# Kernel optimization log

Hardware: AMD Instinct MI355X
Metric: run time of the kernel (lower is better)

## Reference

```python
import jax, jax.numpy as jnp
import numpy as np

T, B, I, H, L, D = 512, 64, 128, 256, 6, 2
G = 3 * H  # gates r, z, n (torch order)


def setup_inputs() -> dict:
    key = jax.random.key(0)
    ks = jax.random.split(key, 10)
    stdv = 1.0 / np.sqrt(H)
    u = lambda k, shp: jax.random.uniform(k, shp, jnp.float32, -stdv, stdv)
    return {
        "x": jax.random.normal(ks[0], (T, B, I), jnp.float32),
        "h0": jax.random.normal(ks[1], (L * D, B, H), jnp.float32),
        "w_ih0": u(ks[2], (D, G, I)),
        "w_hh0": u(ks[3], (D, G, H)),
        "b_ih0": u(ks[4], (D, G)),
        "b_hh0": u(ks[5], (D, G)),
        "w_ihr": u(ks[6], (L - 1, D, G, D * H)),
        "w_hhr": u(ks[7], (L - 1, D, G, H)),
        "b_ihr": u(ks[8], (L - 1, D, G)),
        "b_hhr": u(ks[9], (L - 1, D, G)),
    }


def _gru_direction(xg, h0, w_hh, b_hh, reverse):
    # xg: [T,B,3H] precomputed input-gate projections; h0: [B,H]
    if reverse:
        xg = xg[::-1]

    def step(h, xg_t):
        hg = h @ w_hh.T + b_hh                      # [B,3H]
        xr, xz, xn = jnp.split(xg_t, 3, axis=-1)
        hr, hz, hn = jnp.split(hg, 3, axis=-1)
        r = jax.nn.sigmoid(xr + hr)
        z = jax.nn.sigmoid(xz + hz)
        n = jnp.tanh(xn + r * hn)
        h_new = (1.0 - z) * n + z * h
        return h_new, h_new

    hT, ys = jax.lax.scan(step, h0, xg)
    if reverse:
        ys = ys[::-1]
    return ys, hT


def reference(x, h0, w_ih0, w_hh0, b_ih0, b_hh0, w_ihr, w_hhr, b_ihr, b_hhr):
    out = x
    h_n = []
    for layer in range(L):
        dir_outs = []
        for d in range(D):
            if layer == 0:
                w_ih, w_hh = w_ih0[d], w_hh0[d]
                b_ih, b_hh = b_ih0[d], b_hh0[d]
            else:
                w_ih, w_hh = w_ihr[layer - 1, d], w_hhr[layer - 1, d]
                b_ih, b_hh = b_ihr[layer - 1, d], b_hhr[layer - 1, d]
            # one big GEMM over the whole sequence for the input projection
            xg = jnp.einsum('tbi,gi->tbg', out, w_ih) + b_ih  # [T,B,3H]
            ys, hT = _gru_direction(xg, h0[layer * D + d], w_hh, b_hh,
                                    reverse=(d == 1))
            dir_outs.append(ys)
            h_n.append(hT)
        out = jnp.concatenate(dir_outs, axis=-1)  # [T,B,2H]
    return out, jnp.stack(h_n)  # ([T,B,2H], [L*D,B,H])
```

## Files before the change

kernel.cpp:

```cpp
#include <hip/hip_runtime.h>
#include <hip/hip_fp16.h>

typedef short bf16x8 __attribute__((ext_vector_type(8)));
typedef float f32x4  __attribute__((ext_vector_type(4)));
typedef _Float16 h2_t __attribute__((ext_vector_type(2)));

#define T_ 512
#define B_ 64
#define I_ 128
#define H_ 256
#define L_ 6
#define M_ 32768

static constexpr size_t XG_OFF    = 0;
static constexpr size_t X0_OFF    = 100663296;
static constexpr size_t YA_OFF    = 109051904;
static constexpr size_t YB_OFF    = 142606336;
static constexpr size_t WIH0_OFF  = 176160768;
static constexpr size_t WIHR_OFF  = 176553984;
static constexpr size_t WSCAN_OFF = 184418304;
static constexpr size_t BIAS_OFF  = 189136896;

__global__ void cvt_bf16(const float* __restrict__ s, unsigned short* __restrict__ d, int n) {
  for (int i = blockIdx.x * blockDim.x + threadIdx.x; i < n; i += gridDim.x * blockDim.x) {
    unsigned u = __builtin_bit_cast(unsigned, s[i]);
    u += 0x7fffu + ((u >> 16) & 1u);
    d[i] = (unsigned short)(u >> 16);
  }
}

__global__ void prep_wscan(const float* __restrict__ whh0, const float* __restrict__ whhr,
                           unsigned int* __restrict__ out) {
  int idx = blockIdx.x * 256 + threadIdx.x;
  int ld  = idx / 98304;
  int rem = idx - ld * 98304;
  int tg  = rem >> 15;
  int r   = (rem >> 8) & 127;
  int j   = rem & 255;
  const float* src = (ld < 2) ? (whh0 + (size_t)ld * 196608) : (whhr + (size_t)(ld - 2) * 196608);
  const float* row = src + (size_t)(tg * 256 + j) * 256;
  h2_t p; p[0] = (_Float16)row[2 * r]; p[1] = (_Float16)row[2 * r + 1];
  out[idx] = __builtin_bit_cast(unsigned int, p);
}

__global__ void prep_bias(const float* __restrict__ bih0, const float* __restrict__ bhh0,
                          const float* __restrict__ bihr, const float* __restrict__ bhhr,
                          float* __restrict__ out) {
  int idx = blockIdx.x * 256 + threadIdx.x;
  int ld = idx >> 10;
  int c  = (idx >> 8) & 3;
  int j  = idx & 255;
  const float* bi = (ld < 2) ? bih0 + ld * 768 : bihr + (ld - 2) * 768;
  const float* bh = (ld < 2) ? bhh0 + ld * 768 : bhhr + (ld - 2) * 768;
  float v;
  if (c == 0)      v = bi[j] + bh[j];
  else if (c == 1) v = bi[256 + j] + bh[256 + j];
  else if (c == 2) v = bi[512 + j];
  else             v = bh[512 + j];
  out[idx] = v;
}

__device__ __forceinline__ void llds16(const void* g, void* l) {
  __builtin_amdgcn_global_load_lds((const __attribute__((address_space(1))) void*)g,
                                   (__attribute__((address_space(3))) void*)l, 16, 0, 0);
}

__global__ __launch_bounds__(256)
void gemm_bt(const unsigned short* __restrict__ A,
             const unsigned short* __restrict__ Wl,
             __half* __restrict__ xg,
             int K) {
  const int m0 = blockIdx.x * 128;
  const int n0 = blockIdx.y * 128;
  const int d  = blockIdx.z;
  const unsigned short* W = Wl + (size_t)d * 768 * K;
  __half* C = xg + (size_t)d * M_ * 768;

  __shared__ short As[128 * 64];
  __shared__ short Bs[128 * 64];

  const int tid  = threadIdx.x;
  const int lane = tid & 63;

  const int wv = tid >> 6;
  const int wm = wv >> 1, wn = wv & 1;

  f32x4 acc[4][4] = {};

  for (int kt = 0; kt < K; kt += 64) {
#pragma unroll
    for (int i = 0; i < 4; i++) {
      int e = i * 256 + tid;
      int r = e >> 3, c = (e & 7) << 3;
      llds16(A + (size_t)(m0 + r) * K + kt + c, &As[e * 8]);
    }
#pragma unroll
    for (int i = 0; i < 4; i++) {
      int e = i * 256 + tid;
      int r = e >> 3, c = (e & 7) << 3;
      llds16(W + (size_t)(n0 + r) * K + kt + c, &Bs[e * 8]);
    }
    __syncthreads();
#pragma unroll
    for (int kf = 0; kf < 2; ++kf) {
      bf16x8 a[4], b[4];
      const int krow = kf * 32 + ((lane >> 4) << 3);
#pragma unroll
      for (int f = 0; f < 4; ++f)
        a[f] = *(const bf16x8*)&As[(wm * 64 + f * 16 + (lane & 15)) * 64 + krow];
#pragma unroll
      for (int f = 0; f < 4; ++f)
        b[f] = *(const bf16x8*)&Bs[(wn * 64 + f * 16 + (lane & 15)) * 64 + krow];
#pragma unroll
      for (int i = 0; i < 4; i++)
#pragma unroll
        for (int jn = 0; jn < 4; jn++)
          acc[i][jn] = __builtin_amdgcn_mfma_f32_16x16x32_bf16(a[i], b[jn], acc[i][jn], 0, 0, 0);
    }
    __syncthreads();
  }
#pragma unroll
  for (int i = 0; i < 4; i++) {
    const int row_b = m0 + wm * 64 + i * 16 + ((lane >> 4) << 2);
#pragma unroll
    for (int jn = 0; jn < 4; jn++) {
      const int col = n0 + wn * 64 + jn * 16 + (lane & 15);
#pragma unroll
      for (int v = 0; v < 4; ++v)
        C[(size_t)(row_b + v) * 768 + col] = __float2half(acc[i][jn][v]);
    }
  }
}

#define FDOT2(a, b, c) __builtin_amdgcn_fdot2((a), (b), (c), false)

__device__ __forceinline__ float dpp_xor1(float x) {
  int r = __builtin_amdgcn_update_dpp(0, __builtin_bit_cast(int, x), 0xB1, 0xF, 0xF, true);
  return __builtin_bit_cast(float, r);
}

__global__ __launch_bounds__(512, 2)
void gru_scan2(const unsigned int* __restrict__ wscan,
               const float* __restrict__ bias4,
               const __half* __restrict__ xg,
               const float* __restrict__ h0,
               unsigned short* __restrict__ yout,
               float* __restrict__ dout,
               int layer, int last) {
  const int tid  = threadIdx.x;
  const int j    = tid >> 1;
  const int half = tid & 1;
  const int b    = blockIdx.x;
  const int d    = blockIdx.y;
  const int ld   = layer * 2 + d;

  unsigned int wr[64], wz[64], wn_[64];
  {
    const unsigned int* wb = wscan + (size_t)ld * 98304 + (size_t)half * 64 * 256 + j;
#pragma unroll
    for (int r = 0; r < 64; r++) wr[r]  = wb[r * 256];
#pragma unroll
    for (int r = 0; r < 64; r++) wz[r]  = wb[32768 + r * 256];
#pragma unroll
    for (int r = 0; r < 64; r++) wn_[r] = wb[65536 + r * 256];
  }
  const float* bb = bias4 + ld * 1024;
  const float bR = bb[j], bZ = bb[256 + j], bXn = bb[512 + j], bHn = bb[768 + j];

  __shared__ __attribute__((aligned(16))) unsigned short hb[2][256];

  float h = h0[(size_t)ld * 16384 + b * 256 + j];
  if (half == 0) hb[0][j] = __half_as_ushort(__float2half(h));

  const __half* xgd = xg + (size_t)d * M_ * 768;
  const int t0 = d ? 511 : 0;
  size_t xb = (size_t)(t0 * 64 + b) * 768 + j;
  __half cxr = xgd[xb], cxz = xgd[xb + 256], cxn = xgd[xb + 512];

  __syncthreads();

  for (int s = 0; s < 512; s++) {
    const int cur = s & 1;
    const int sn = (s + 1) & 511;
    const int t1 = d ? 511 - sn : sn;
    const size_t xb1 = (size_t)(t1 * 64 + b) * 768 + j;
    const __half nxr = xgd[xb1], nxz = xgd[xb1 + 256], nxn = xgd[xb1 + 512];

    float ar = 0.f, az = 0.f, an = 0.f;
    const uint4* hp = (const uint4*)(&hb[cur][half << 7]);
#pragma unroll
    for (int q = 0; q < 16; q++) {
      const uint4 hv = hp[q];
      const h2_t p0 = __builtin_bit_cast(h2_t, hv.x);
      const h2_t p1 = __builtin_bit_cast(h2_t, hv.y);
      const h2_t p2 = __builtin_bit_cast(h2_t, hv.z);
      const h2_t p3 = __builtin_bit_cast(h2_t, hv.w);
      ar = FDOT2(p0, __builtin_bit_cast(h2_t, wr[4 * q + 0]), ar);
      az = FDOT2(p0, __builtin_bit_cast(h2_t, wz[4 * q + 0]), az);
      an = FDOT2(p0, __builtin_bit_cast(h2_t, wn_[4 * q + 0]), an);
      ar = FDOT2(p1, __builtin_bit_cast(h2_t, wr[4 * q + 1]), ar);
      az = FDOT2(p1, __builtin_bit_cast(h2_t, wz[4 * q + 1]), az);
      an = FDOT2(p1, __builtin_bit_cast(h2_t, wn_[4 * q + 1]), an);
      ar = FDOT2(p2, __builtin_bit_cast(h2_t, wr[4 * q + 2]), ar);
      az = FDOT2(p2, __builtin_bit_cast(h2_t, wz[4 * q + 2]), az);
      an = FDOT2(p2, __builtin_bit_cast(h2_t, wn_[4 * q + 2]), an);
      ar = FDOT2(p3, __builtin_bit_cast(h2_t, wr[4 * q + 3]), ar);
      az = FDOT2(p3, __builtin_bit_cast(h2_t, wz[4 * q + 3]), az);
      an = FDOT2(p3, __builtin_bit_cast(h2_t, wn_[4 * q + 3]), an);
    }
    ar += dpp_xor1(ar);
    az += dpp_xor1(az);
    an += dpp_xor1(an);

    const float prer = ar + __half2float(cxr) + bR;
    const float prez = az + __half2float(cxz) + bZ;
    const float r = __builtin_amdgcn_rcpf(1.f + __builtin_amdgcn_exp2f(-1.44269504f * prer));
    const float z = __builtin_amdgcn_rcpf(1.f + __builtin_amdgcn_exp2f(-1.44269504f * prez));
    const float pren = __half2float(cxn) + bXn + r * (an + bHn);
    const float e2 = __builtin_amdgcn_exp2f(2.88539008f * pren);
    const float n = 1.f - 2.f * __builtin_amdgcn_rcpf(e2 + 1.f);
    h = n + z * (h - n);

    if (half == 0) {
      hb[cur ^ 1][j] = __half_as_ushort(__float2half(h));
      const int t = d ? 511 - s : s;
      const size_t orow = (size_t)(t * 64 + b) * 512 + (size_t)d * 256 + j;
      if (last) {
        dout[orow] = h;
      } else {
        unsigned u = __builtin_bit_cast(unsigned, h);
        u += 0x7fffu + ((u >> 16) & 1u);
        yout[orow] = (unsigned short)(u >> 16);
      }
    }
    cxr = nxr; cxz = nxz; cxn = nxn;
    __syncthreads();
  }
  if (half == 0) dout[16777216 + (size_t)ld * 16384 + b * 256 + j] = h;
}

extern "C" void kernel_launch(void* const* d_in, const int* in_sizes, int n_in,
                              void* d_out, int out_size, void* d_ws, size_t ws_size,
                              hipStream_t stream) {
  const float* x    = (const float*)d_in[0];
  const float* h0   = (const float*)d_in[1];
  const float* wih0 = (const float*)d_in[2];
  const float* whh0 = (const float*)d_in[3];
  const float* bih0 = (const float*)d_in[4];
  const float* bhh0 = (const float*)d_in[5];
  const float* wihr = (const float*)d_in[6];
  const float* whhr = (const float*)d_in[7];
  const float* bihr = (const float*)d_in[8];
  const float* bhhr = (const float*)d_in[9];

  char* ws = (char*)d_ws;
  __half*        xg    = (__half*)(ws + XG_OFF);
  unsigned short* x0   = (unsigned short*)(ws + X0_OFF);
  unsigned short* yA   = (unsigned short*)(ws + YA_OFF);
  unsigned short* yB   = (unsigned short*)(ws + YB_OFF);
  unsigned short* wih0b= (unsigned short*)(ws + WIH0_OFF);
  unsigned short* wihrb= (unsigned short*)(ws + WIHR_OFF);
  unsigned int*  wscan = (unsigned int*)(ws + WSCAN_OFF);
  float*         bias4 = (float*)(ws + BIAS_OFF);
  float*         dout  = (float*)d_out;

  cvt_bf16<<<4096, 256, 0, stream>>>(x, x0, M_ * I_);
  cvt_bf16<<<768, 256, 0, stream>>>(wih0, wih0b, 2 * 768 * 128);
  cvt_bf16<<<4096, 256, 0, stream>>>(wihr, wihrb, 5 * 2 * 768 * 512);
  prep_wscan<<<4608, 256, 0, stream>>>(whh0, whhr, wscan);
  prep_bias<<<48, 256, 0, stream>>>(bih0, bhh0, bihr, bhhr, bias4);

  for (int l = 0; l < L_; l++) {
    unsigned short* yw = (l & 1) ? yB : yA;
    const unsigned short* A = (l == 0) ? x0 : ((l & 1) ? yA : yB);
    const int K = (l == 0) ? 128 : 512;
    const unsigned short* W = (l == 0) ? wih0b : wihrb + (size_t)(l - 1) * 2 * 768 * 512;

    gemm_bt<<<dim3(256, 6, 2), 256, 0, stream>>>(A, W, xg, K);
    gru_scan2<<<dim3(64, 2), 512, 0, stream>>>(wscan, bias4, xg, h0, yw, dout, l, l == L_ - 1);
  }
}
```

Before: 3.802 ms.

## Split recurrent weights between LDS and registers in GRU scan kernel

The recurrent weight slice per thread was held entirely in 192 VGPRs. It now keeps 40 rows per gate in registers and puts the first 24 rows per gate (144KB) in LDS. The hidden-state buffer is also XOR-swizzled so the two halves of a thread pair read different LDS banks. Launch bounds drop to one block per CU to match the LDS footprint. The aim is to cut register pressure or spilling in the serial time loop, at the cost of extra LDS reads on every step.

```diff
diff --git a/kernel.cpp b/kernel.cpp
--- a/kernel.cpp
+++ b/kernel.cpp
@@ -133,13 +133,14 @@
 }
 
 #define FDOT2(a, b, c) __builtin_amdgcn_fdot2((a), (b), (c), false)
+#define BC2(u) __builtin_bit_cast(h2_t, (u))
 
 __device__ __forceinline__ float dpp_xor1(float x) {
   int r = __builtin_amdgcn_update_dpp(0, __builtin_bit_cast(int, x), 0xB1, 0xF, 0xF, true);
   return __builtin_bit_cast(float, r);
 }
 
-__global__ __launch_bounds__(512, 2)
+__global__ __launch_bounds__(512, 1)
 void gru_scan2(const unsigned int* __restrict__ wscan,
                const float* __restrict__ bias4,
                const __half* __restrict__ xg,
@@ -154,30 +155,51 @@
   const int d    = blockIdx.y;
   const int ld   = layer * 2 + d;
 
-  unsigned int wr[64], wz[64], wn_[64];
-  {
-    const unsigned int* wb = wscan + (size_t)ld * 98304 + (size_t)half * 64 * 256 + j;
-#pragma unroll
-    for (int r = 0; r < 64; r++) wr[r]  = wb[r * 256];
-#pragma unroll
-    for (int r = 0; r < 64; r++) wz[r]  = wb[32768 + r * 256];
-#pragma unroll
-    for (int r = 0; r < 64; r++) wn_[r] = wb[65536 + r * 256];
-  }
+  __shared__ unsigned int wlds[36864];
+  __shared__ __attribute__((aligned(16))) char hbc[2][512];
+
+  const unsigned int* wb = wscan + (size_t)ld * 98304 + (size_t)half * 16384 + j;
+
+#pragma unroll
+  for (int g = 0; g < 3; g++)
+#pragma unroll
+    for (int rr = 0; rr < 24; rr++)
+      wlds[g * 12288 + rr * 512 + tid] = wb[g * 32768 + rr * 256];
+
+  unsigned int wr[40], wz[40], wn_[40];
+#pragma unroll
+  for (int i = 0; i < 40; i++) wr[i]  = wb[(24 + i) * 256];
+#pragma unroll
+  for (int i = 0; i < 40; i++) wz[i]  = wb[32768 + (24 + i) * 256];
+#pragma unroll
+  for (int i = 0; i < 40; i++) wn_[i] = wb[65536 + (24 + i) * 256];
+#pragma unroll
+  for (int i = 0; i < 40; i++) {
+    asm volatile("" : "+v"(wr[i]));
+    asm volatile("" : "+v"(wz[i]));
+    asm volatile("" : "+v"(wn_[i]));
+  }
+
   const float* bb = bias4 + ld * 1024;
   const float bR = bb[j], bZ = bb[256 + j], bXn = bb[512 + j], bHn = bb[768 + j];
 
-  __shared__ __attribute__((aligned(16))) unsigned short hb[2][256];
+  const int wboff = (j * 2) ^ ((j & 128) >> 3);
 
   float h = h0[(size_t)ld * 16384 + b * 256 + j];
-  if (half == 0) hb[0][j] = __half_as_ushort(__float2half(h));
+  if (half == 0) *(unsigned short*)(hbc[0] + wboff) = __half_as_ushort(__float2half(h));
 
   const __half* xgd = xg + (size_t)d * M_ * 768;
   const int t0 = d ? 511 : 0;
   size_t xb = (size_t)(t0 * 64 + b) * 768 + j;
   __half cxr = xgd[xb], cxz = xgd[xb + 256], cxn = xgd[xb + 512];
 
+  const int halfoff = half << 8;
+  int tb = tid;
+
   __syncthreads();
+
+#define RD(k) (*(const uint4*)(rb + halfoff + ((((k) ^ half)) << 4)))
+#define AFENCE asm volatile("" : "+v"(ar), "+v"(az), "+v"(an) :: "memory")
 
   for (int s = 0; s < 512; s++) {
     const int cur = s & 1;
@@ -186,28 +208,38 @@
     const size_t xb1 = (size_t)(t1 * 64 + b) * 768 + j;
     const __half nxr = xgd[xb1], nxz = xgd[xb1 + 256], nxn = xgd[xb1 + 512];
 
+    asm volatile("" : "+v"(tb));
+
     float ar = 0.f, az = 0.f, an = 0.f;
-    const uint4* hp = (const uint4*)(&hb[cur][half << 7]);
-#pragma unroll
-    for (int q = 0; q < 16; q++) {
-      const uint4 hv = hp[q];
-      const h2_t p0 = __builtin_bit_cast(h2_t, hv.x);
-      const h2_t p1 = __builtin_bit_cast(h2_t, hv.y);
-      const h2_t p2 = __builtin_bit_cast(h2_t, hv.z);
-      const h2_t p3 = __builtin_bit_cast(h2_t, hv.w);
-      ar = FDOT2(p0, __builtin_bit_cast(h2_t, wr[4 * q + 0]), ar);
-      az = FDOT2(p0, __builtin_bit_cast(h2_t, wz[4 * q + 0]), az);
-      an = FDOT2(p0, __builtin_bit_cast(h2_t, wn_[4 * q + 0]), an);
-      ar = FDOT2(p1, __builtin_bit_cast(h2_t, wr[4 * q + 1]), ar);
-      az = FDOT2(p1, __builtin_bit_cast(h2_t, wz[4 * q + 1]), az);
-      an = FDOT2(p1, __builtin_bit_cast(h2_t, wn_[4 * q + 1]), an);
-      ar = FDOT2(p2, __builtin_bit_cast(h2_t, wr[4 * q + 2]), ar);
-      az = FDOT2(p2, __builtin_bit_cast(h2_t, wz[4 * q + 2]), az);
-      an = FDOT2(p2, __builtin_bit_cast(h2_t, wn_[4 * q + 2]), an);
-      ar = FDOT2(p3, __builtin_bit_cast(h2_t, wr[4 * q + 3]), ar);
-      az = FDOT2(p3, __builtin_bit_cast(h2_t, wz[4 * q + 3]), az);
-      an = FDOT2(p3, __builtin_bit_cast(h2_t, wn_[4 * q + 3]), an);
-    }
+    const char* rb = hbc[cur];
+
+#pragma unroll
+    for (int q = 0; q < 6; q++) {
+      const uint4 hv = RD(q);
+#pragma unroll
+      for (int e = 0; e < 4; e++) {
+        const unsigned he = (&hv.x)[e];
+        const int rr = q * 4 + e;
+        ar = FDOT2(BC2(he), BC2(wlds[rr * 512 + tb]), ar);
+        az = FDOT2(BC2(he), BC2(wlds[12288 + rr * 512 + tb]), az);
+        an = FDOT2(BC2(he), BC2(wlds[24576 + rr * 512 + tb]), an);
+      }
+      if (q & 1) AFENCE;
+    }
+#pragma unroll
+    for (int q = 6; q < 16; q++) {
+      const uint4 hv = RD(q);
+#pragma unroll
+      for (int e = 0; e < 4; e++) {
+        const unsigned he = (&hv.x)[e];
+        const int i = (q - 6) * 4 + e;
+        ar = FDOT2(BC2(he), BC2(wr[i]), ar);
+        az = FDOT2(BC2(he), BC2(wz[i]), az);
+        an = FDOT2(BC2(he), BC2(wn_[i]), an);
+      }
+      if (q & 1) AFENCE;
+    }
+
     ar += dpp_xor1(ar);
     az += dpp_xor1(az);
     an += dpp_xor1(an);
@@ -222,7 +254,7 @@
     h = n + z * (h - n);
 
     if (half == 0) {
-      hb[cur ^ 1][j] = __half_as_ushort(__float2half(h));
+      *(unsigned short*)(hbc[cur ^ 1] + wboff) = __half_as_ushort(__float2half(h));
       const int t = d ? 511 - s : s;
       const size_t orow = (size_t)(t * 64 + b) * 512 + (size_t)d * 256 + j;
       if (last) {
@@ -236,6 +268,8 @@
     cxr = nxr; cxz = nxz; cxn = nxn;
     __syncthreads();
   }
+#undef RD
+#undef AFENCE
   if (half == 0) dout[16777216 + (size_t)ld * 16384 + b * 256 + j] = h;
 }
 
```

Result: slower. 5.347 ms (+40.6%).
